# Kernel optimization log

Measured on AMD Instinct MI355X. Metric: run time of the kernel, lower is better.

The kernel has to match this reference:

```python
import jax, jax.numpy as jnp
import numpy as np

GLYPH_DIM = 4096
PADDING_IDX = GLYPH_DIM  # 4096
GLYPH_EMB = 20           # CHAR_EMB 16 + COLOR_EMB 4
HIDDEN = 32
MAX_LEN = 64


def setup_inputs() -> dict:
    key = jax.random.key(0)
    k1, k2, k3, k4, k5, k6, k7 = jax.random.split(key, 7)
    B, H, W = 8192, 21, 79
    glyph_chars = jax.random.randint(k1, (B, H, W), 0, 256, dtype=jnp.int32)
    glyph_colors = jax.random.randint(k2, (B, H, W), 0, 16, dtype=jnp.int32)
    # Embedding table with zero padding row (torch padding_idx semantics)
    emb_table = jax.random.normal(k3, (GLYPH_DIM + 1, GLYPH_EMB), dtype=jnp.float32) * 0.02
    emb_table = emb_table.at[PADDING_IDX].set(0.0)
    s = 1.0 / np.sqrt(HIDDEN)
    W_ih = jax.random.uniform(k4, (HIDDEN, GLYPH_EMB), minval=-s, maxval=s, dtype=jnp.float32)
    W_hh = jax.random.uniform(k5, (HIDDEN, HIDDEN), minval=-s, maxval=s, dtype=jnp.float32)
    b_ih = jax.random.uniform(k6, (HIDDEN,), minval=-s, maxval=s, dtype=jnp.float32)
    b_hh = jax.random.uniform(k7, (HIDDEN,), minval=-s, maxval=s, dtype=jnp.float32)
    return {"glyph_chars": glyph_chars, "glyph_colors": glyph_colors,
            "emb_table": emb_table, "W_ih": W_ih, "W_hh": W_hh,
            "b_ih": b_ih, "b_hh": b_hh}


def _encode_bag(glyph_chars, glyph_colors):
    """Batched sorted-unique compaction over the bounded glyph id range."""
    B = glyph_chars.shape[0]
    g_ids = ((glyph_chars << 4) + glyph_colors).reshape(B, -1)  # [B, H*W]
    # presence[b, g] = glyph g appears in sample b (batched histogram)
    bidx = jnp.broadcast_to(jnp.arange(B, dtype=g_ids.dtype)[:, None], g_ids.shape)
    presence = jnp.zeros((B, GLYPH_DIM), dtype=bool).at[bidx, g_ids].set(True)
    # compact: present ids keep their value, absent become PADDING_IDX (=4096),
    # so sorting yields ascending unique ids followed by padding.
    ids = jnp.arange(GLYPH_DIM, dtype=jnp.int32)
    keys = jnp.where(presence, ids, jnp.int32(PADDING_IDX))
    bag = jnp.sort(keys, axis=1)[:, :MAX_LEN]  # [B, MAX_LEN]
    lengths = jnp.minimum(presence.sum(axis=1), MAX_LEN)  # [B]
    return bag, lengths


def reference(glyph_chars, glyph_colors, emb_table, W_ih, W_hh, b_ih, b_hh):
    bag, lengths = _encode_bag(glyph_chars, glyph_colors)
    emb = emb_table[bag]  # [B, MAX_LEN, GLYPH_EMB]
    B = emb.shape[0]

    # packed RNN == plain RNN where hidden state freezes past each sequence length
    xs = jnp.swapaxes(emb, 0, 1)  # [T, B, E]

    def step(h, inp):
        xt, t = inp
        h_new = jnp.tanh(xt @ W_ih.T + b_ih + h @ W_hh.T + b_hh)
        h = jnp.where((t < lengths)[:, None], h_new, h)
        return h, None

    h0 = jnp.zeros((B, HIDDEN), dtype=emb.dtype)
    h, _ = jax.lax.scan(step, h0, (xs, jnp.arange(MAX_LEN)))
    return (h, emb, bag)
```

## Files before the change

kernel.cpp:

```cpp
#include <hip/hip_runtime.h>

#define HW 1659
#define PADID 4096
#define EMB 20
#define HID 32
#define MAXLEN 64

__global__ __launch_bounds__(128) void proj_kernel(
    const float* __restrict__ emb_table, const float* __restrict__ W_ih,
    float* __restrict__ proj)
{
    const int tid = threadIdx.x;
    const int g = blockIdx.x * 4 + (tid >> 5);
    const int j = tid & 31;
    if (g > PADID) return;
    const float* er = emb_table + (size_t)g * EMB;
    const float* wr = W_ih + j * EMB;
    float s = 0.f;
#pragma unroll
    for (int k = 0; k < EMB; k++) s += wr[k] * er[k];
    proj[(size_t)g * HID + j] = s;
}

__global__ __launch_bounds__(256) void bag_emb_kernel(
    const int* __restrict__ chars, const int* __restrict__ colors,
    const float* __restrict__ emb_table,
    float* __restrict__ out_emb, float* __restrict__ out_bag)
{
    __shared__ unsigned char pres[4096];
    __shared__ int bagl[64];
    __shared__ int wsum[4];

    const int b   = blockIdx.x;
    const int tid = threadIdx.x;
    const int lane = tid & 63;
    const int wv   = tid >> 6;

    ((uint4*)pres)[tid] = make_uint4(0u, 0u, 0u, 0u);
    if (tid < 64) bagl[tid] = PADID;
    __syncthreads();

    const int base = b * HW;
    const int pe = (4 - (base & 3)) & 3;
    if (tid < pe) {
        int g = (chars[base + tid] << 4) + colors[base + tid];
        pres[g] = 1;
    }
    const int nv = (HW - pe) >> 2;
    const int nt = HW - pe - (nv << 2);
    const int4* c4 = (const int4*)(chars + base + pe);
    const int4* k4 = (const int4*)(colors + base + pe);
    for (int v = tid; v < nv; v += 256) {
        int4 c = c4[v], k = k4[v];
        pres[(c.x << 4) + k.x] = 1;
        pres[(c.y << 4) + k.y] = 1;
        pres[(c.z << 4) + k.z] = 1;
        pres[(c.w << 4) + k.w] = 1;
    }
    if (tid < nt) {
        int i = base + pe + (nv << 2) + tid;
        pres[(chars[i] << 4) + colors[i]] = 1;
    }
    __syncthreads();

    uint4 w4 = ((const uint4*)pres)[tid];
    const unsigned M = 0x01010101u;
    int cnt = __popc(w4.x & M) + __popc(w4.y & M)
            + __popc(w4.z & M) + __popc(w4.w & M);

    int pre = cnt;
#pragma unroll
    for (int d = 1; d < 64; d <<= 1) {
        int v = __shfl_up(pre, d, 64);
        if (lane >= d) pre += v;
    }
    if (lane == 63) wsum[wv] = pre;
    __syncthreads();
    int wbase = 0;
#pragma unroll
    for (int w2 = 0; w2 < 4; w2++) wbase += (w2 < wv) ? wsum[w2] : 0;
    int p = wbase + pre - cnt;

    unsigned wrd[4] = {w4.x, w4.y, w4.z, w4.w};
#pragma unroll
    for (int c = 0; c < 4; c++) {
#pragma unroll
        for (int k = 0; k < 4; k++) {
            if ((wrd[c] >> (8 * k)) & 1) {
                if (p < 64) bagl[p] = 16 * tid + 4 * c + k;
                p++;
            }
        }
    }
    __syncthreads();

    if (tid < 64) out_bag[(size_t)b * 64 + tid] = (float)bagl[tid];

    const float4* tab4 = (const float4*)emb_table;
    float4* dst4 = (float4*)(out_emb + (size_t)b * (MAXLEN * EMB));
    for (int q = tid; q < MAXLEN * 5; q += 256) {
        int t = q / 5;
        int m = q - t * 5;
        int row = bagl[t];
        dst4[q] = tab4[row * 5 + m];
    }
}

__global__ __launch_bounds__(128, 4) void rnn_kernel(
    const float* __restrict__ proj, const float* __restrict__ bagf,
    const float* __restrict__ W_hh,
    const float* __restrict__ b_ih, const float* __restrict__ b_hh,
    float* __restrict__ out_h)
{
    __shared__ float hbuf[8][32];

    const int tid  = threadIdx.x;
    const int wv   = tid >> 6;
    const int lane = tid & 63;
    const int sl   = lane >> 4;
    const int ib   = wv * 4 + sl;
    const int jj   = lane & 15;
    const int b    = blockIdx.x * 8 + ib;

    float w0[HID], w1[HID];
#pragma unroll
    for (int k = 0; k < HID; k++) {
        const int src = ((k & 1) << 4) + (k >> 1);
        w0[k] = W_hh[jj * HID + src];
        w1[k] = W_hh[(jj + 16) * HID + src];
    }
    const float sb0 = b_ih[jj] + b_hh[jj];
    const float sb1 = b_ih[jj + 16] + b_hh[jj + 16];

    const float* bps = bagf + (size_t)b * 64;

    unsigned long long mm0 = __ballot(bps[jj]      < 4095.5f);
    unsigned long long mm1 = __ballot(bps[jj + 16] < 4095.5f);
    unsigned long long mm2 = __ballot(bps[jj + 32] < 4095.5f);
    unsigned long long mm3 = __ballot(bps[jj + 48] < 4095.5f);
    const int sh = sl * 16;
    const int len = __popc((unsigned)((mm0 >> sh) & 0xFFFFu))
                  + __popc((unsigned)((mm1 >> sh) & 0xFFFFu))
                  + __popc((unsigned)((mm2 >> sh) & 0xFFFFu))
                  + __popc((unsigned)((mm3 >> sh) & 0xFFFFu));

    ((float2*)hbuf[ib])[jj] = make_float2(0.f, 0.f);
    asm volatile("s_waitcnt lgkmcnt(0)" ::: "memory");

    float h0 = 0.f, h1 = 0.f;
    for (int t = 0; t < MAXLEN; t++) {
        const int idx = (int)bps[t];
        const float pv0 = proj[idx * HID + jj];
        const float pv1 = proj[idx * HID + jj + 16];

        const float4* hb4 = (const float4*)hbuf[ib];
        float a0 = sb0 + pv0, a1 = sb1 + pv1, c0 = 0.f, c1 = 0.f;
#pragma unroll
        for (int m = 0; m < 8; m += 2) {
            float4 u = hb4[m], v = hb4[m + 1];
            a0 += w0[4*m+0]*u.x + w0[4*m+1]*u.y + w0[4*m+2]*u.z + w0[4*m+3]*u.w;
            a1 += w1[4*m+0]*u.x + w1[4*m+1]*u.y + w1[4*m+2]*u.z + w1[4*m+3]*u.w;
            c0 += w0[4*m+4]*v.x + w0[4*m+5]*v.y + w0[4*m+6]*v.z + w0[4*m+7]*v.w;
            c1 += w1[4*m+4]*v.x + w1[4*m+5]*v.y + w1[4*m+6]*v.z + w1[4*m+7]*v.w;
        }
        float s0 = a0 + c0, s1 = a1 + c1;

        s0 = fminf(fmaxf(s0, -9.f), 9.f);
        s1 = fminf(fmaxf(s1, -9.f), 9.f);
        float e0 = __expf(2.f * s0);
        float e1 = __expf(2.f * s1);
        float th0 = (e0 - 1.f) * __builtin_amdgcn_rcpf(e0 + 1.f);
        float th1 = (e1 - 1.f) * __builtin_amdgcn_rcpf(e1 + 1.f);

        h0 = (t < len) ? th0 : h0;
        h1 = (t < len) ? th1 : h1;

        ((float2*)hbuf[ib])[jj] = make_float2(h0, h1);
        asm volatile("s_waitcnt lgkmcnt(0)" ::: "memory");
    }

    out_h[(size_t)b * HID + jj]      = h0;
    out_h[(size_t)b * HID + jj + 16] = h1;
}

__global__ __launch_bounds__(128, 4) void rnn_kernel_noproj(
    const float* __restrict__ emb, const float* __restrict__ bagf,
    const float* __restrict__ W_ih, const float* __restrict__ W_hh,
    const float* __restrict__ b_ih, const float* __restrict__ b_hh,
    float* __restrict__ out_h)
{
    __shared__ float hbuf[4][32];
    const int tid = threadIdx.x;
    const int ib  = tid >> 5;
    const int j   = tid & 31;
    const int b   = blockIdx.x * 4 + ib;

    float wih[EMB];
#pragma unroll
    for (int k = 0; k < EMB; k++) wih[k] = W_ih[j * EMB + k];
    float whh[HID];
#pragma unroll
    for (int k = 0; k < HID; k++) whh[k] = W_hh[j * HID + k];
    const float sbias = b_ih[j] + b_hh[j];

    const float* bp = bagf + (size_t)b * 64;
    unsigned long long m0 = __ballot(bp[j]      < 4095.5f);
    unsigned long long m1 = __ballot(bp[32 + j] < 4095.5f);
    const int half = ib & 1;
    const int len = __popc((unsigned)(m0 >> (half * 32)))
                  + __popc((unsigned)(m1 >> (half * 32)));

    hbuf[ib][j] = 0.f;
    asm volatile("s_waitcnt lgkmcnt(0)" ::: "memory");

    float h = 0.f;
    const float* xb = emb + (size_t)b * (MAXLEN * EMB);
    for (int t = 0; t < MAXLEN; t++) {
        const float4* xp = (const float4*)(xb + t * EMB);
        float4 x0 = xp[0], x1 = xp[1], x2 = xp[2], x3 = xp[3], x4 = xp[4];
        float s = sbias;
        const float4* hb4 = (const float4*)hbuf[ib];
#pragma unroll
        for (int m = 0; m < 8; m++) {
            float4 hv = hb4[m];
            s += whh[4*m+0]*hv.x + whh[4*m+1]*hv.y
               + whh[4*m+2]*hv.z + whh[4*m+3]*hv.w;
        }
        s += wih[0]*x0.x + wih[1]*x0.y + wih[2]*x0.z + wih[3]*x0.w;
        s += wih[4]*x1.x + wih[5]*x1.y + wih[6]*x1.z + wih[7]*x1.w;
        s += wih[8]*x2.x + wih[9]*x2.y + wih[10]*x2.z + wih[11]*x2.w;
        s += wih[12]*x3.x + wih[13]*x3.y + wih[14]*x3.z + wih[15]*x3.w;
        s += wih[16]*x4.x + wih[17]*x4.y + wih[18]*x4.z + wih[19]*x4.w;
        s = fminf(fmaxf(s, -9.f), 9.f);
        float e = __expf(2.f * s);
        float th = (e - 1.f) * __builtin_amdgcn_rcpf(e + 1.f);
        h = (t < len) ? th : h;
        hbuf[ib][j] = h;
        asm volatile("s_waitcnt lgkmcnt(0)" ::: "memory");
    }
    out_h[(size_t)b * HID + j] = h;
}

extern "C" void kernel_launch(void* const* d_in, const int* in_sizes, int n_in,
                              void* d_out, int out_size, void* d_ws, size_t ws_size,
                              hipStream_t stream) {
    const int*   chars     = (const int*)d_in[0];
    const int*   colors    = (const int*)d_in[1];
    const float* emb_table = (const float*)d_in[2];
    const float* W_ih      = (const float*)d_in[3];
    const float* W_hh      = (const float*)d_in[4];
    const float* b_ih      = (const float*)d_in[5];
    const float* b_hh      = (const float*)d_in[6];

    const int B = in_sizes[0] / HW;

    float* out     = (float*)d_out;
    float* out_h   = out;
    float* out_emb = out + (size_t)B * HID;
    float* out_bag = out_emb + (size_t)B * MAXLEN * EMB;

    const size_t proj_bytes = (size_t)(PADID + 1) * HID * sizeof(float);

    bag_emb_kernel<<<B, 256, 0, stream>>>(chars, colors, emb_table, out_emb, out_bag);

    if (ws_size >= proj_bytes) {
        float* proj = (float*)d_ws;
        proj_kernel<<<(PADID + 1 + 3) / 4, 128, 0, stream>>>(emb_table, W_ih, proj);
        rnn_kernel<<<B / 8, 128, 0, stream>>>(proj, out_bag, W_hh, b_ih, b_hh, out_h);
    } else {
        rnn_kernel_noproj<<<B / 4, 128, 0, stream>>>(out_emb, out_bag, W_ih, W_hh,
                                                     b_ih, b_hh, out_h);
    }
}
```

Before: 194.5 us.

## Use one wavefront per sample in bag kernel and pipeline RNN gathers

The bag/embedding kernel now handles four samples per block, one 64-lane wavefront each, with a private presence array per wave. This drops all block barriers, and a permuted presence index lets each lane scan 64 contiguous glyph ids. The RNN kernel prefetches the projected-input rows two timesteps ahead, uses packed v2f FMAs for the recurrent matvec, and computes tanh as 1-2/(e+1) without the clamp. Each wave now walks the whole 1659-element sample alone, so per-sample latency goes up, and dropping the clamp changes how tanh behaves at extreme values.

```diff
diff --git a/kernel.cpp b/kernel.cpp
--- a/kernel.cpp
+++ b/kernel.cpp
@@ -5,6 +5,8 @@
 #define EMB 20
 #define HID 32
 #define MAXLEN 64
+
+typedef float v2f __attribute__((ext_vector_type(2)));
 
 __global__ __launch_bounds__(128) void proj_kernel(
     const float* __restrict__ emb_table, const float* __restrict__ W_ih,
@@ -27,81 +29,88 @@
     const float* __restrict__ emb_table,
     float* __restrict__ out_emb, float* __restrict__ out_bag)
 {
-    __shared__ unsigned char pres[4096];
-    __shared__ int bagl[64];
-    __shared__ int wsum[4];
-
-    const int b   = blockIdx.x;
-    const int tid = threadIdx.x;
+    __shared__ unsigned char pres[4][4096];
+    __shared__ int bagl[4][64];
+
+    const int tid  = threadIdx.x;
+    const int wv   = tid >> 6;
     const int lane = tid & 63;
-    const int wv   = tid >> 6;
-
-    ((uint4*)pres)[tid] = make_uint4(0u, 0u, 0u, 0u);
-    if (tid < 64) bagl[tid] = PADID;
-    __syncthreads();
+    const int b    = blockIdx.x * 4 + wv;
+
+    unsigned char* pr = pres[wv];
+    uint4* pz = (uint4*)pr;
+#pragma unroll
+    for (int i = 0; i < 4; i++) pz[lane + 64 * i] = make_uint4(0u, 0u, 0u, 0u);
+    bagl[wv][lane] = PADID;
+    asm volatile("s_waitcnt lgkmcnt(0)" ::: "memory");
 
     const int base = b * HW;
     const int pe = (4 - (base & 3)) & 3;
-    if (tid < pe) {
-        int g = (chars[base + tid] << 4) + colors[base + tid];
-        pres[g] = 1;
+    if (lane < pe) {
+        int g = (chars[base + lane] << 4) + colors[base + lane];
+        pr[((g & 0x30) << 6) | ((g >> 6) << 4) | (g & 15)] = 1;
     }
     const int nv = (HW - pe) >> 2;
     const int nt = HW - pe - (nv << 2);
     const int4* c4 = (const int4*)(chars + base + pe);
     const int4* k4 = (const int4*)(colors + base + pe);
-    for (int v = tid; v < nv; v += 256) {
+    for (int v = lane; v < nv; v += 64) {
         int4 c = c4[v], k = k4[v];
-        pres[(c.x << 4) + k.x] = 1;
-        pres[(c.y << 4) + k.y] = 1;
-        pres[(c.z << 4) + k.z] = 1;
-        pres[(c.w << 4) + k.w] = 1;
-    }
-    if (tid < nt) {
-        int i = base + pe + (nv << 2) + tid;
-        pres[(chars[i] << 4) + colors[i]] = 1;
-    }
-    __syncthreads();
-
-    uint4 w4 = ((const uint4*)pres)[tid];
+        int g0 = (c.x << 4) + k.x, g1 = (c.y << 4) + k.y;
+        int g2 = (c.z << 4) + k.z, g3 = (c.w << 4) + k.w;
+        pr[((g0 & 0x30) << 6) | ((g0 >> 6) << 4) | (g0 & 15)] = 1;
+        pr[((g1 & 0x30) << 6) | ((g1 >> 6) << 4) | (g1 & 15)] = 1;
+        pr[((g2 & 0x30) << 6) | ((g2 >> 6) << 4) | (g2 & 15)] = 1;
+        pr[((g3 & 0x30) << 6) | ((g3 >> 6) << 4) | (g3 & 15)] = 1;
+    }
+    if (lane < nt) {
+        int i = base + pe + (nv << 2) + lane;
+        int g = (chars[i] << 4) + colors[i];
+        pr[((g & 0x30) << 6) | ((g >> 6) << 4) | (g & 15)] = 1;
+    }
+    asm volatile("s_waitcnt lgkmcnt(0)" ::: "memory");
+
+    uint4 q0 = pz[lane], q1 = pz[lane + 64], q2 = pz[lane + 128], q3 = pz[lane + 192];
     const unsigned M = 0x01010101u;
-    int cnt = __popc(w4.x & M) + __popc(w4.y & M)
-            + __popc(w4.z & M) + __popc(w4.w & M);
-
+    int cnt = __popc(q0.x & M) + __popc(q0.y & M) + __popc(q0.z & M) + __popc(q0.w & M)
+            + __popc(q1.x & M) + __popc(q1.y & M) + __popc(q1.z & M) + __popc(q1.w & M)
+            + __popc(q2.x & M) + __popc(q2.y & M) + __popc(q2.z & M) + __popc(q2.w & M)
+            + __popc(q3.x & M) + __popc(q3.y & M) + __popc(q3.z & M) + __popc(q3.w & M);
     int pre = cnt;
 #pragma unroll
     for (int d = 1; d < 64; d <<= 1) {
         int v = __shfl_up(pre, d, 64);
         if (lane >= d) pre += v;
     }
-    if (lane == 63) wsum[wv] = pre;
-    __syncthreads();
-    int wbase = 0;
-#pragma unroll
-    for (int w2 = 0; w2 < 4; w2++) wbase += (w2 < wv) ? wsum[w2] : 0;
-    int p = wbase + pre - cnt;
-
-    unsigned wrd[4] = {w4.x, w4.y, w4.z, w4.w};
-#pragma unroll
-    for (int c = 0; c < 4; c++) {
-#pragma unroll
-        for (int k = 0; k < 4; k++) {
-            if ((wrd[c] >> (8 * k)) & 1) {
-                if (p < 64) bagl[p] = 16 * tid + 4 * c + k;
-                p++;
+    int p = pre - cnt;
+
+    if (p < 64) {
+        unsigned wrd[16] = {q0.x, q0.y, q0.z, q0.w, q1.x, q1.y, q1.z, q1.w,
+                            q2.x, q2.y, q2.z, q2.w, q3.x, q3.y, q3.z, q3.w};
+#pragma unroll
+        for (int w = 0; w < 16; w++) {
+            unsigned x = wrd[w];
+#pragma unroll
+            for (int k = 0; k < 4; k++) {
+                if ((x >> (8 * k)) & 1) {
+                    if (p < 64) bagl[wv][p] = 64 * lane + 4 * w + k;
+                    p++;
+                }
             }
         }
     }
-    __syncthreads();
-
-    if (tid < 64) out_bag[(size_t)b * 64 + tid] = (float)bagl[tid];
+    asm volatile("s_waitcnt lgkmcnt(0)" ::: "memory");
+
+    out_bag[(size_t)b * 64 + lane] = (float)bagl[wv][lane];
 
     const float4* tab4 = (const float4*)emb_table;
     float4* dst4 = (float4*)(out_emb + (size_t)b * (MAXLEN * EMB));
-    for (int q = tid; q < MAXLEN * 5; q += 256) {
+#pragma unroll
+    for (int it = 0; it < 5; it++) {
+        int q = lane + 64 * it;
         int t = q / 5;
-        int m = q - t * 5;
-        int row = bagl[t];
+        int m = q - 5 * t;
+        int row = bagl[wv][t];
         dst4[q] = tab4[row * 5 + m];
     }
 }
@@ -122,14 +131,13 @@
     const int jj   = lane & 15;
     const int b    = blockIdx.x * 8 + ib;
 
-    float w0[HID], w1[HID];
-#pragma unroll
-    for (int k = 0; k < HID; k++) {
-        const int src = ((k & 1) << 4) + (k >> 1);
-        w0[k] = W_hh[jj * HID + src];
-        w1[k] = W_hh[(jj + 16) * HID + src];
-    }
-    const float sb0 = b_ih[jj] + b_hh[jj];
+    v2f w0p[16], w1p[16];
+#pragma unroll
+    for (int m = 0; m < 16; m++) {
+        w0p[m] = (v2f){W_hh[jj * HID + 2*m], W_hh[jj * HID + 2*m + 1]};
+        w1p[m] = (v2f){W_hh[(jj+16) * HID + 2*m], W_hh[(jj+16) * HID + 2*m + 1]};
+    }
+    const float sb0 = b_ih[jj]      + b_hh[jj];
     const float sb1 = b_ih[jj + 16] + b_hh[jj + 16];
 
     const float* bps = bagf + (size_t)b * 64;
@@ -144,39 +152,56 @@
                   + __popc((unsigned)((mm2 >> sh) & 0xFFFFu))
                   + __popc((unsigned)((mm3 >> sh) & 0xFFFFu));
 
-    ((float2*)hbuf[ib])[jj] = make_float2(0.f, 0.f);
-    asm volatile("s_waitcnt lgkmcnt(0)" ::: "memory");
+    hbuf[ib][jj]      = 0.f;
+    hbuf[ib][jj + 16] = 0.f;
+    asm volatile("s_waitcnt lgkmcnt(0)" ::: "memory");
+
+    int   idxB = (int)bps[0];
+    int   idxC = (int)bps[1];
+    float pv0 = proj[idxB * HID + jj];
+    float pv1 = proj[idxB * HID + jj + 16];
 
     float h0 = 0.f, h1 = 0.f;
     for (int t = 0; t < MAXLEN; t++) {
-        const int idx = (int)bps[t];
-        const float pv0 = proj[idx * HID + jj];
-        const float pv1 = proj[idx * HID + jj + 16];
+        const int t2 = (t + 2 < MAXLEN) ? (t + 2) : (MAXLEN - 1);
+        const int idxD = (int)bps[t2];
+        const float pv0n = proj[idxC * HID + jj];
+        const float pv1n = proj[idxC * HID + jj + 16];
 
         const float4* hb4 = (const float4*)hbuf[ib];
-        float a0 = sb0 + pv0, a1 = sb1 + pv1, c0 = 0.f, c1 = 0.f;
+        v2f a0 = (v2f){0.f, 0.f}, a1 = a0, c0 = a0, c1 = a0;
 #pragma unroll
         for (int m = 0; m < 8; m += 2) {
             float4 u = hb4[m], v = hb4[m + 1];
-            a0 += w0[4*m+0]*u.x + w0[4*m+1]*u.y + w0[4*m+2]*u.z + w0[4*m+3]*u.w;
-            a1 += w1[4*m+0]*u.x + w1[4*m+1]*u.y + w1[4*m+2]*u.z + w1[4*m+3]*u.w;
-            c0 += w0[4*m+4]*v.x + w0[4*m+5]*v.y + w0[4*m+6]*v.z + w0[4*m+7]*v.w;
-            c1 += w1[4*m+4]*v.x + w1[4*m+5]*v.y + w1[4*m+6]*v.z + w1[4*m+7]*v.w;
+            v2f ulo = (v2f){u.x, u.y}, uhi = (v2f){u.z, u.w};
+            v2f vlo = (v2f){v.x, v.y}, vhi = (v2f){v.z, v.w};
+            a0 = __builtin_elementwise_fma(w0p[2*m],     ulo, a0);
+            a0 = __builtin_elementwise_fma(w0p[2*m + 1], uhi, a0);
+            a1 = __builtin_elementwise_fma(w1p[2*m],     ulo, a1);
+            a1 = __builtin_elementwise_fma(w1p[2*m + 1], uhi, a1);
+            c0 = __builtin_elementwise_fma(w0p[2*m + 2], vlo, c0);
+            c0 = __builtin_elementwise_fma(w0p[2*m + 3], vhi, c0);
+            c1 = __builtin_elementwise_fma(w1p[2*m + 2], vlo, c1);
+            c1 = __builtin_elementwise_fma(w1p[2*m + 3], vhi, c1);
         }
-        float s0 = a0 + c0, s1 = a1 + c1;
-
-        s0 = fminf(fmaxf(s0, -9.f), 9.f);
-        s1 = fminf(fmaxf(s1, -9.f), 9.f);
+        v2f t0 = a0 + c0;
+        v2f t1 = a1 + c1;
+        float s0 = sb0 + pv0 + t0.x + t0.y;
+        float s1 = sb1 + pv1 + t1.x + t1.y;
+
         float e0 = __expf(2.f * s0);
         float e1 = __expf(2.f * s1);
-        float th0 = (e0 - 1.f) * __builtin_amdgcn_rcpf(e0 + 1.f);
-        float th1 = (e1 - 1.f) * __builtin_amdgcn_rcpf(e1 + 1.f);
+        float th0 = 1.f - 2.f * __builtin_amdgcn_rcpf(e0 + 1.f);
+        float th1 = 1.f - 2.f * __builtin_amdgcn_rcpf(e1 + 1.f);
 
         h0 = (t < len) ? th0 : h0;
         h1 = (t < len) ? th1 : h1;
 
-        ((float2*)hbuf[ib])[jj] = make_float2(h0, h1);
+        hbuf[ib][jj]      = h0;
+        hbuf[ib][jj + 16] = h1;
         asm volatile("s_waitcnt lgkmcnt(0)" ::: "memory");
+
+        pv0 = pv0n; pv1 = pv1n; idxC = idxD;
     }
 
     out_h[(size_t)b * HID + jj]      = h0;
@@ -261,7 +286,7 @@
 
     const size_t proj_bytes = (size_t)(PADID + 1) * HID * sizeof(float);
 
-    bag_emb_kernel<<<B, 256, 0, stream>>>(chars, colors, emb_table, out_emb, out_bag);
+    bag_emb_kernel<<<B / 4, 256, 0, stream>>>(chars, colors, emb_table, out_emb, out_bag);
 
     if (ws_size >= proj_bytes) {
         float* proj = (float*)d_ws;
```

Result: no change. 193.1 us (-0.7%).
